# Optimization experiments

Hardware: AMD Instinct MI355X
Metric: run time of the kernel (lower is better)

Reference implementation:

```python
import jax, jax.numpy as jnp
import numpy as np

B, T, I, H = 64, 1024, 128, 512

def setup_inputs() -> dict:
    key = jax.random.key(0)
    ks = jax.random.split(key, 7)
    s_ih = 1.0 / np.sqrt(H)
    return {
        "x": jax.random.normal(ks[0], (B, T, I), dtype=jnp.float32),
        "W_ih": jax.random.uniform(ks[1], (H, I), minval=-s_ih, maxval=s_ih, dtype=jnp.float32),
        "W_hh": jax.random.uniform(ks[2], (H, H), minval=-s_ih, maxval=s_ih, dtype=jnp.float32),
        "b_ih": jax.random.uniform(ks[3], (H,), minval=-s_ih, maxval=s_ih, dtype=jnp.float32),
        "b_hh": jax.random.uniform(ks[4], (H,), minval=-s_ih, maxval=s_ih, dtype=jnp.float32),
        "fc_w": jax.random.uniform(ks[5], (1, H), minval=-s_ih, maxval=s_ih, dtype=jnp.float32),
        "fc_b": jax.random.uniform(ks[6], (1,), minval=-s_ih, maxval=s_ih, dtype=jnp.float32),
    }

def reference(x, W_ih, W_hh, b_ih, b_hh, fc_w, fc_b):
    # Precompute input projection for all timesteps: [B,T,H]
    xp = jnp.einsum('bti,hi->bth', x, W_ih) + b_ih + b_hh

    def step(h, xp_t):
        # h: [B,H], xp_t: [B,H]
        h_new = jnp.tanh(xp_t + h @ W_hh.T)
        return h_new, None

    h0 = jnp.zeros((B, H), dtype=x.dtype)
    h_last, _ = jax.lax.scan(step, h0, jnp.swapaxes(xp, 0, 1))  # scan over T
    # final linear head: [B,1]
    return h_last @ fc_w.T + fc_b
```

## Files before the change

### kernel.cpp

```cpp
#include <hip/hip_runtime.h>
#include <math.h>

#define B_ 64
#define T_ 1024
#define I_ 128
#define H_ 512

typedef _Float16 h2_t __attribute__((ext_vector_type(2)));
union U32H2 { unsigned u; h2_t h; };

__device__ __forceinline__ float fdot2u(unsigned a, unsigned b, float c) {
    U32H2 ua, ub; ua.u = a; ub.u = b;
    return __builtin_amdgcn_fdot2(ua.h, ub.h, c, false);
}
__device__ __forceinline__ unsigned packh2(float x, float y) {
    U32H2 r; r.h.x = (_Float16)x; r.h.y = (_Float16)y; return r.u;
}

__global__ void prep(const float* __restrict__ wih, const float* __restrict__ whh,
                     const float* __restrict__ bih, const float* __restrict__ bhh,
                     unsigned* __restrict__ wpack, unsigned* __restrict__ wldsg,
                     unsigned* __restrict__ wih2, float* __restrict__ biasv) {
    int e = blockIdx.x * 256 + threadIdx.x;
    if (e < 98304) {
        int u4 = e >> 2, r4 = e & 3;
        int qr = u4 >> 10, tid = u4 & 1023;
        int r = qr / 6, q = qr % 6;
        int m = (q << 2) + r4;
        int c = tid >> 7, g = tid & 127;
        int j = (g << 2) + r;
        int w = (c << 5) + m;
        wpack[e] = packh2(whh[j * H_ + 2 * w], whh[j * H_ + 2 * w + 1]);
    }
    if (e < 32768) {
        int u = e >> 2, r = e & 3;
        int c = u >> 10, mp = (u >> 7) & 7, g = u & 127;
        int j = (g << 2) + r;
        int w = (c << 5) + 24 + mp;
        wldsg[e] = packh2(whh[j * H_ + 2 * w], whh[j * H_ + 2 * w + 1]);
    }
    if (e < 64 * 512) {
        int i2 = e >> 9, h = e & 511;
        wih2[e] = packh2(wih[h * I_ + (i2 << 1)], wih[h * I_ + (i2 << 1) + 1]);
    }
    if (e < H_) biasv[e] = bih[e] + bhh[e];
}

__global__ __launch_bounds__(512, 2) void xp_gemm(
    const float* __restrict__ x, const unsigned* __restrict__ wih2,
    const float* __restrict__ biasv, _Float16* __restrict__ xph) {
    __shared__ unsigned w2[64 * 512];
    __shared__ unsigned x2[32 * 64];
    const int tid = threadIdx.x, b = blockIdx.x, t0 = blockIdx.y * 32;

    #pragma unroll
    for (int q = 0; q < 64; ++q) w2[tid + (q << 9)] = wih2[tid + (q << 9)];
    #pragma unroll
    for (int q = 0; q < 4; ++q) {
        int idx = tid * 4 + q;
        int t = idx >> 6, i2 = idx & 63;
        const float2 xv = *(const float2*)(x + ((size_t)b * T_ + t0 + t) * I_ + (i2 << 1));
        x2[idx] = packh2(xv.x, xv.y);
    }
    __syncthreads();
    const float bias = biasv[tid];
    for (int t = 0; t < 32; ++t) {
        float acc = bias;
        #pragma unroll
        for (int i2 = 0; i2 < 64; ++i2)
            acc = fdot2u(x2[(t << 6) + i2], w2[(i2 << 9) + tid], acc);
        xph[((size_t)b * T_ + t0 + t) * H_ + tid] = (_Float16)acc;
    }
}

__global__ __launch_bounds__(1024) void rnn_fused(
    const unsigned* __restrict__ xp2,
    const unsigned* __restrict__ wpack,
    const unsigned* __restrict__ wldsg,
    const float* __restrict__ fcw, const float* __restrict__ fcb,
    float* __restrict__ out)
{
    __shared__ __align__(16) unsigned wlds[32768];
    __shared__ __align__(16) float part[8 * 512];
    __shared__ __align__(16) unsigned h2buf[256];
    __shared__ float wsum[4];

    const int tid = threadIdx.x;
    const int b = blockIdx.x;
    const int c = tid >> 7, g = tid & 127;

    {
        const uint4* src = (const uint4*)wldsg;
        uint4* dst = (uint4*)wlds;
        #pragma unroll
        for (int q = 0; q < 8; ++q) dst[tid + (q << 10)] = src[tid + (q << 10)];
    }
    uint4 wr[4][6];
    {
        const uint4* wp4 = ((const uint4*)wpack) + tid;
        #pragma unroll
        for (int r = 0; r < 4; ++r)
            #pragma unroll
            for (int q = 0; q < 6; ++q)
                wr[r][q] = wp4[(r * 6 + q) << 10];
    }
    if (tid < 256) h2buf[tid] = 0u;
    __syncthreads();

    const unsigned* xpb = xp2 + (size_t)b * T_ * 256;
    const uint4* hv  = ((const uint4*)h2buf) + (c << 3);
    const uint4* wqp = ((const uint4*)wlds) + (c << 10) + g;
    float4* pw = ((float4*)part) + (c << 7) + g;
    const float2* p2 = (const float2*)part;

    unsigned xpw = (tid < 256) ? xpb[tid] : 0u;

    for (int t = 0; t < T_; ++t) {
        unsigned xpn = (tid < 256) ? xpb[(t + 1) * 256 + tid] : 0u;

        float a0 = 0.f, a1 = 0.f, a2 = 0.f, a3 = 0.f;
        #pragma unroll
        for (int q = 0; q < 6; ++q) {
            const uint4 hh = hv[q];
            a0 = fdot2u(wr[0][q].x, hh.x, a0); a1 = fdot2u(wr[1][q].x, hh.x, a1);
            a2 = fdot2u(wr[2][q].x, hh.x, a2); a3 = fdot2u(wr[3][q].x, hh.x, a3);
            a0 = fdot2u(wr[0][q].y, hh.y, a0); a1 = fdot2u(wr[1][q].y, hh.y, a1);
            a2 = fdot2u(wr[2][q].y, hh.y, a2); a3 = fdot2u(wr[3][q].y, hh.y, a3);
            a0 = fdot2u(wr[0][q].z, hh.z, a0); a1 = fdot2u(wr[1][q].z, hh.z, a1);
            a2 = fdot2u(wr[2][q].z, hh.z, a2); a3 = fdot2u(wr[3][q].z, hh.z, a3);
            a0 = fdot2u(wr[0][q].w, hh.w, a0); a1 = fdot2u(wr[1][q].w, hh.w, a1);
            a2 = fdot2u(wr[2][q].w, hh.w, a2); a3 = fdot2u(wr[3][q].w, hh.w, a3);
        }
        #pragma unroll
        for (int q = 0; q < 2; ++q) {
            const uint4 hh = hv[6 + q];
            {   const uint4 w0 = wqp[(q * 4 + 0) * 128];
                a0 = fdot2u(w0.x, hh.x, a0); a1 = fdot2u(w0.y, hh.x, a1);
                a2 = fdot2u(w0.z, hh.x, a2); a3 = fdot2u(w0.w, hh.x, a3); }
            {   const uint4 w1 = wqp[(q * 4 + 1) * 128];
                a0 = fdot2u(w1.x, hh.y, a0); a1 = fdot2u(w1.y, hh.y, a1);
                a2 = fdot2u(w1.z, hh.y, a2); a3 = fdot2u(w1.w, hh.y, a3); }
            {   const uint4 w2v = wqp[(q * 4 + 2) * 128];
                a0 = fdot2u(w2v.x, hh.z, a0); a1 = fdot2u(w2v.y, hh.z, a1);
                a2 = fdot2u(w2v.z, hh.z, a2); a3 = fdot2u(w2v.w, hh.z, a3); }
            {   const uint4 w3 = wqp[(q * 4 + 3) * 128];
                a0 = fdot2u(w3.x, hh.w, a0); a1 = fdot2u(w3.y, hh.w, a1);
                a2 = fdot2u(w3.z, hh.w, a2); a3 = fdot2u(w3.w, hh.w, a3); }
        }
        *pw = make_float4(a0, a1, a2, a3);
        __syncthreads();

        if (tid < 256) {
            float sx = 0.f, sy = 0.f;
            #pragma unroll
            for (int cc = 0; cc < 8; ++cc) {
                const float2 s = p2[(cc << 8) + tid];
                sx += s.x; sy += s.y;
            }
            U32H2 xu; xu.u = xpw;
            float pre0 = (float)xu.h.x + sx;
            float pre1 = (float)xu.h.y + sy;
            float e0 = __expf(2.0f * pre0), e1 = __expf(2.0f * pre1);
            float h0 = 1.0f - 2.0f / (e0 + 1.0f);
            float h1 = 1.0f - 2.0f / (e1 + 1.0f);
            h2buf[tid] = packh2(h0, h1);
        }
        xpw = xpn;
        __syncthreads();
    }

    float p = 0.f;
    if (tid < 256) {
        U32H2 hu; hu.u = h2buf[tid];
        p = (float)hu.h.x * fcw[tid << 1] + (float)hu.h.y * fcw[(tid << 1) + 1];
    }
    #pragma unroll
    for (int off = 32; off >= 1; off >>= 1) p += __shfl_down(p, off, 64);
    if ((tid & 63) == 0 && tid < 256) wsum[tid >> 6] = p;
    __syncthreads();
    if (tid == 0) out[b] = wsum[0] + wsum[1] + wsum[2] + wsum[3] + fcb[0];
}

extern "C" void kernel_launch(void* const* d_in, const int* in_sizes, int n_in,
                              void* d_out, int out_size, void* d_ws, size_t ws_size,
                              hipStream_t stream) {
    const float* x   = (const float*)d_in[0];
    const float* wih = (const float*)d_in[1];
    const float* whh = (const float*)d_in[2];
    const float* bih = (const float*)d_in[3];
    const float* bhh = (const float*)d_in[4];
    const float* fcw = (const float*)d_in[5];
    const float* fcb = (const float*)d_in[6];
    float* out = (float*)d_out;

    unsigned* xp2   = (unsigned*)d_ws;
    unsigned* wpack = xp2 + 16777216;
    unsigned* wldsg = wpack + 98304;
    unsigned* wih2  = wldsg + 32768;
    float*    biasv = (float*)(wih2 + 32768);

    hipLaunchKernelGGL(prep, dim3(384), dim3(256), 0, stream,
                       wih, whh, bih, bhh, wpack, wldsg, wih2, biasv);
    hipLaunchKernelGGL(xp_gemm, dim3(B_, 32), dim3(512), 0, stream,
                       x, wih2, biasv, (_Float16*)xp2);
    hipLaunchKernelGGL(rnn_fused, dim3(B_), dim3(1024), 0, stream,
                       xp2, wpack, wldsg, fcw, fcb, out);
}
```

Baseline: 1.762 ms.

## Halve RNN block size, reduce partials via wave shuffles, double-buffer hidden state

The recurrent kernel drops from 1024 to 512 threads. Each thread now holds 52 of 64 weight words per row in registers, with the rest in LDS. The cross-split reduction moves from an LDS partial buffer to in-wave xor shuffles, so every lane computes the tanh itself. The hidden state is double-buffered, which leaves one barrier per timestep instead of two. This raises register pressure (208 VGPRs of weights) and puts more dot-product work on each thread, in exchange for less LDS traffic and fewer syncs on the serial critical path.

```diff
diff --git a/kernel.cpp b/kernel.cpp
--- a/kernel.cpp
+++ b/kernel.cpp
@@ -22,22 +22,27 @@
                      unsigned* __restrict__ wpack, unsigned* __restrict__ wldsg,
                      unsigned* __restrict__ wih2, float* __restrict__ biasv) {
     int e = blockIdx.x * 256 + threadIdx.x;
-    if (e < 98304) {
-        int u4 = e >> 2, r4 = e & 3;
-        int qr = u4 >> 10, tid = u4 & 1023;
-        int r = qr / 6, q = qr % 6;
-        int m = (q << 2) + r4;
-        int c = tid >> 7, g = tid & 127;
-        int j = (g << 2) + r;
-        int w = (c << 5) + m;
-        wpack[e] = packh2(whh[j * H_ + 2 * w], whh[j * H_ + 2 * w + 1]);
-    }
-    if (e < 32768) {
-        int u = e >> 2, r = e & 3;
-        int c = u >> 10, mp = (u >> 7) & 7, g = u & 127;
-        int j = (g << 2) + r;
-        int w = (c << 5) + 24 + mp;
-        wldsg[e] = packh2(whh[j * H_ + 2 * w], whh[j * H_ + 2 * w + 1]);
+    if (e < 106496) {
+        int r4 = e & 3;
+        int u4 = e >> 2;
+        int tid = u4 & 511;
+        int jq = u4 >> 9;
+        int j = jq / 13, q = jq % 13;
+        int c = (tid >> 4) & 3;
+        int g = ((tid >> 6) << 4) + (tid & 15);
+        int row = (g << 2) + j;
+        int word = (c << 6) + (q << 2) + r4;
+        wpack[e] = packh2(whh[row * H_ + 2 * word], whh[row * H_ + 2 * word + 1]);
+    }
+    if (e < 24576) {
+        int r = e & 3;
+        int uu = e >> 2;
+        int g = uu & 127;
+        int cm = uu >> 7;
+        int c = cm / 12, m = cm % 12;
+        int row = (g << 2) + r;
+        int word = (c << 6) + 52 + m;
+        wldsg[e] = packh2(whh[row * H_ + 2 * word], whh[row * H_ + 2 * word + 1]);
     }
     if (e < 64 * 512) {
         int i2 = e >> 9, h = e & 511;
@@ -73,54 +78,54 @@
     }
 }
 
-__global__ __launch_bounds__(1024) void rnn_fused(
+__global__ __launch_bounds__(512) void rnn_fused(
     const unsigned* __restrict__ xp2,
     const unsigned* __restrict__ wpack,
     const unsigned* __restrict__ wldsg,
     const float* __restrict__ fcw, const float* __restrict__ fcb,
     float* __restrict__ out)
 {
-    __shared__ __align__(16) unsigned wlds[32768];
-    __shared__ __align__(16) float part[8 * 512];
-    __shared__ __align__(16) unsigned h2buf[256];
+    __shared__ __align__(16) unsigned wlds[24576];
+    __shared__ __align__(16) unsigned h2buf[512];
     __shared__ float wsum[4];
 
     const int tid = threadIdx.x;
     const int b = blockIdx.x;
-    const int c = tid >> 7, g = tid & 127;
+    const int l = tid & 63;
+    const int w = tid >> 6;
+    const int u = l & 15;
+    const int c = (l >> 4) & 3;
+    const int g = (w << 4) + u;
 
     {
         const uint4* src = (const uint4*)wldsg;
         uint4* dst = (uint4*)wlds;
         #pragma unroll
-        for (int q = 0; q < 8; ++q) dst[tid + (q << 10)] = src[tid + (q << 10)];
-    }
-    uint4 wr[4][6];
+        for (int q = 0; q < 12; ++q) dst[tid + (q << 9)] = src[tid + (q << 9)];
+    }
+    uint4 wr[4][13];
     {
         const uint4* wp4 = ((const uint4*)wpack) + tid;
         #pragma unroll
-        for (int r = 0; r < 4; ++r)
+        for (int j = 0; j < 4; ++j)
             #pragma unroll
-            for (int q = 0; q < 6; ++q)
-                wr[r][q] = wp4[(r * 6 + q) << 10];
+            for (int q = 0; q < 13; ++q)
+                wr[j][q] = wp4[(j * 13 + q) << 9];
     }
     if (tid < 256) h2buf[tid] = 0u;
     __syncthreads();
 
     const unsigned* xpb = xp2 + (size_t)b * T_ * 256;
-    const uint4* hv  = ((const uint4*)h2buf) + (c << 3);
-    const uint4* wqp = ((const uint4*)wlds) + (c << 10) + g;
-    float4* pw = ((float4*)part) + (c << 7) + g;
-    const float2* p2 = (const float2*)part;
-
-    unsigned xpw = (tid < 256) ? xpb[tid] : 0u;
+    const uint4* wq = ((const uint4*)wlds) + c * 1536 + g;
 
     for (int t = 0; t < T_; ++t) {
-        unsigned xpn = (tid < 256) ? xpb[(t + 1) * 256 + tid] : 0u;
+        const int p = t & 1;
+        const uint4* hv = ((const uint4*)(h2buf + (p << 8))) + (c << 4);
+        const uint2 xpw = *(const uint2*)(xpb + t * 256 + 2 * g);
 
         float a0 = 0.f, a1 = 0.f, a2 = 0.f, a3 = 0.f;
         #pragma unroll
-        for (int q = 0; q < 6; ++q) {
+        for (int q = 0; q < 13; ++q) {
             const uint4 hh = hv[q];
             a0 = fdot2u(wr[0][q].x, hh.x, a0); a1 = fdot2u(wr[1][q].x, hh.x, a1);
             a2 = fdot2u(wr[2][q].x, hh.x, a2); a3 = fdot2u(wr[3][q].x, hh.x, a3);
@@ -132,51 +137,50 @@
             a2 = fdot2u(wr[2][q].w, hh.w, a2); a3 = fdot2u(wr[3][q].w, hh.w, a3);
         }
         #pragma unroll
-        for (int q = 0; q < 2; ++q) {
-            const uint4 hh = hv[6 + q];
-            {   const uint4 w0 = wqp[(q * 4 + 0) * 128];
+        for (int s = 0; s < 3; ++s) {
+            const uint4 hh = hv[13 + s];
+            {   const uint4 w0 = wq[(4 * s + 0) * 128];
                 a0 = fdot2u(w0.x, hh.x, a0); a1 = fdot2u(w0.y, hh.x, a1);
                 a2 = fdot2u(w0.z, hh.x, a2); a3 = fdot2u(w0.w, hh.x, a3); }
-            {   const uint4 w1 = wqp[(q * 4 + 1) * 128];
+            {   const uint4 w1 = wq[(4 * s + 1) * 128];
                 a0 = fdot2u(w1.x, hh.y, a0); a1 = fdot2u(w1.y, hh.y, a1);
                 a2 = fdot2u(w1.z, hh.y, a2); a3 = fdot2u(w1.w, hh.y, a3); }
-            {   const uint4 w2v = wqp[(q * 4 + 2) * 128];
+            {   const uint4 w2v = wq[(4 * s + 2) * 128];
                 a0 = fdot2u(w2v.x, hh.z, a0); a1 = fdot2u(w2v.y, hh.z, a1);
                 a2 = fdot2u(w2v.z, hh.z, a2); a3 = fdot2u(w2v.w, hh.z, a3); }
-            {   const uint4 w3 = wqp[(q * 4 + 3) * 128];
+            {   const uint4 w3 = wq[(4 * s + 3) * 128];
                 a0 = fdot2u(w3.x, hh.w, a0); a1 = fdot2u(w3.y, hh.w, a1);
                 a2 = fdot2u(w3.z, hh.w, a2); a3 = fdot2u(w3.w, hh.w, a3); }
         }
-        *pw = make_float4(a0, a1, a2, a3);
+        a0 += __shfl_xor(a0, 16); a0 += __shfl_xor(a0, 32);
+        a1 += __shfl_xor(a1, 16); a1 += __shfl_xor(a1, 32);
+        a2 += __shfl_xor(a2, 16); a2 += __shfl_xor(a2, 32);
+        a3 += __shfl_xor(a3, 16); a3 += __shfl_xor(a3, 32);
+
+        U32H2 x0, x1; x0.u = xpw.x; x1.u = xpw.y;
+        const float p0 = (float)x0.h.x + a0;
+        const float p1 = (float)x0.h.y + a1;
+        const float p2f = (float)x1.h.x + a2;
+        const float p3 = (float)x1.h.y + a3;
+        const float h0 = 1.f - 2.f * __builtin_amdgcn_rcpf(__expf(2.f * p0) + 1.f);
+        const float h1 = 1.f - 2.f * __builtin_amdgcn_rcpf(__expf(2.f * p1) + 1.f);
+        const float h2v = 1.f - 2.f * __builtin_amdgcn_rcpf(__expf(2.f * p2f) + 1.f);
+        const float h3 = 1.f - 2.f * __builtin_amdgcn_rcpf(__expf(2.f * p3) + 1.f);
+        if (l < 16) {
+            uint2 hw; hw.x = packh2(h0, h1); hw.y = packh2(h2v, h3);
+            *(uint2*)(h2buf + ((p ^ 1) << 8) + 2 * g) = hw;
+        }
         __syncthreads();
-
-        if (tid < 256) {
-            float sx = 0.f, sy = 0.f;
-            #pragma unroll
-            for (int cc = 0; cc < 8; ++cc) {
-                const float2 s = p2[(cc << 8) + tid];
-                sx += s.x; sy += s.y;
-            }
-            U32H2 xu; xu.u = xpw;
-            float pre0 = (float)xu.h.x + sx;
-            float pre1 = (float)xu.h.y + sy;
-            float e0 = __expf(2.0f * pre0), e1 = __expf(2.0f * pre1);
-            float h0 = 1.0f - 2.0f / (e0 + 1.0f);
-            float h1 = 1.0f - 2.0f / (e1 + 1.0f);
-            h2buf[tid] = packh2(h0, h1);
-        }
-        xpw = xpn;
-        __syncthreads();
-    }
-
-    float p = 0.f;
+    }
+
+    float pr = 0.f;
     if (tid < 256) {
         U32H2 hu; hu.u = h2buf[tid];
-        p = (float)hu.h.x * fcw[tid << 1] + (float)hu.h.y * fcw[(tid << 1) + 1];
+        pr = (float)hu.h.x * fcw[tid << 1] + (float)hu.h.y * fcw[(tid << 1) + 1];
     }
     #pragma unroll
-    for (int off = 32; off >= 1; off >>= 1) p += __shfl_down(p, off, 64);
-    if ((tid & 63) == 0 && tid < 256) wsum[tid >> 6] = p;
+    for (int off = 32; off >= 1; off >>= 1) pr += __shfl_down(pr, off, 64);
+    if ((tid & 63) == 0 && tid < 256) wsum[tid >> 6] = pr;
     __syncthreads();
     if (tid == 0) out[b] = wsum[0] + wsum[1] + wsum[2] + wsum[3] + fcb[0];
 }
@@ -195,14 +199,14 @@
 
     unsigned* xp2   = (unsigned*)d_ws;
     unsigned* wpack = xp2 + 16777216;
-    unsigned* wldsg = wpack + 98304;
-    unsigned* wih2  = wldsg + 32768;
+    unsigned* wldsg = wpack + 106496;
+    unsigned* wih2  = wldsg + 24576;
     float*    biasv = (float*)(wih2 + 32768);
 
-    hipLaunchKernelGGL(prep, dim3(384), dim3(256), 0, stream,
+    hipLaunchKernelGGL(prep, dim3(416), dim3(256), 0, stream,
                        wih, whh, bih, bhh, wpack, wldsg, wih2, biasv);
     hipLaunchKernelGGL(xp_gemm, dim3(B_, 32), dim3(512), 0, stream,
                        x, wih2, biasv, (_Float16*)xp2);
-    hipLaunchKernelGGL(rnn_fused, dim3(B_), dim3(1024), 0, stream,
+    hipLaunchKernelGGL(rnn_fused, dim3(B_), dim3(512), 0, stream,
                        xp2, wpack, wldsg, fcw, fcb, out);
 }
```

New measurement: 1.868 ms. 1.06x slower.
